# Kernel optimization log

Measured on AMD Instinct MI355X. Metric: run time of the kernel, lower is better.

Reference implementation:

```python
import jax, jax.numpy as jnp
import numpy as np

B = 8192
H_IN = 128
H = 512
Z = 128
N = 512   # must equal H due to W_up(h,h) -> W_down(n,.) chaining in the source
RW = 16
TEMP = 0.666
EPS = 1e-20


def _xavier(key, shape):
    fan_in, fan_out = shape[0], shape[1]
    lim = float(np.sqrt(6.0 / (fan_in + fan_out)))
    return jax.random.uniform(key, shape, jnp.float32, -lim, lim)


def setup_inputs() -> dict:
    key = jax.random.key(0)
    ks = jax.random.split(key, 24)
    inp = {
        'latent': jax.random.normal(ks[0], (B, Z), jnp.float32),
        'inputs': jnp.zeros((B, H_IN), jnp.float32),
        'gumbel_u': jax.random.uniform(ks[1], (RW, B, N), jnp.float32),
        # weights stored [in, out] for x @ W
        'W_int': _xavier(ks[2], (Z, H)),   'b_int': jnp.zeros((H,), jnp.float32),
        'W_intl': _xavier(ks[3], (Z, H)),  'b_intl': jnp.zeros((H,), jnp.float32),
        'W_hup': _xavier(ks[4], (H, H)),   'b_hup': jnp.zeros((H,), jnp.float32),
        'W_cup': _xavier(ks[5], (H, H)),   'b_cup': jnp.zeros((H,), jnp.float32),
        'W_hupl': _xavier(ks[6], (H, H)),  'b_hupl': jnp.zeros((H,), jnp.float32),
        'W_cupl': _xavier(ks[7], (H, H)),  'b_cupl': jnp.zeros((H,), jnp.float32),
        'W_lstm': _xavier(ks[8], (H_IN + H, 4 * H)), 'b_lstm': jnp.zeros((4 * H,), jnp.float32),
        'W_up': _xavier(ks[9], (H, H)),    'b_up': jnp.zeros((H,), jnp.float32),
        'W_down': _xavier(ks[10], (N, H_IN)),        # no bias
        'W_downl': _xavier(ks[11], (N, H_IN)),       # no bias
        'W_outl': _xavier(ks[12], (H, 1)), 'b_outl': jnp.zeros((1,), jnp.float32),
    }
    return inp


def _lstm_step(x, hx, cx, W_lstm, b_lstm):
    gates = jnp.concatenate([x, hx], axis=1) @ W_lstm + b_lstm  # [B, 4H]
    i, g, f, o = jnp.split(gates, 4, axis=1)
    cy = cx * jax.nn.sigmoid(f + 1.0) + jax.nn.sigmoid(i) * jnp.tanh(g)
    hy = jax.nn.sigmoid(o) * jnp.tanh(cy)
    return hy, cy


def _forward(latent, inputs, gumbel_u,
             W_int, b_int, W_intl, b_intl,
             W_hup, b_hup, W_cup, b_cup,
             W_hupl, b_hupl, W_cupl, b_cupl,
             W_lstm, b_lstm, W_up, b_up,
             W_down, W_downl, W_outl, b_outl):
    inter = jnp.tanh(latent @ W_int + b_int)
    hx = jnp.tanh(inter @ W_hup + b_hup)
    cx = jnp.tanh(inter @ W_cup + b_cup)
    inter_l = jnp.tanh(latent @ W_intl + b_intl)
    hxl = jnp.tanh(inter_l @ W_hupl + b_hupl)
    cxl = jnp.tanh(inter_l @ W_cupl + b_cupl)

    def step1(carry, u):
        x, h, c = carry
        hy, cy = _lstm_step(x, h, c, W_lstm, b_lstm)
        logits = hy @ W_up + b_up                       # [B, N]
        g = -jnp.log(-jnp.log(u + EPS) + EPS)           # gumbel noise
        y = jax.nn.softmax((logits + g) / TEMP, axis=1)
        y_hard = (y == jnp.max(y, axis=1, keepdims=True)).astype(y.dtype)
        y = jax.lax.stop_gradient(y_hard - y) + y       # straight-through hard sample
        return (y @ W_down, hy, cy), y

    _, out_steps = jax.lax.scan(step1, (inputs, hx, cx), gumbel_u)  # [RW, B, N]

    def step2(carry, y):
        h, c = carry
        xl = y @ W_downl
        hy, cy = _lstm_step(xl, h, c, W_lstm, b_lstm)   # source reuses lstm_cell here
        return (hy, cy), hy @ W_outl + b_outl           # [B, 1]

    _, line_steps = jax.lax.scan(step2, (hxl, cxl), out_steps)      # [RW, B, 1]

    return (jnp.transpose(out_steps, (1, 0, 2)),   # [B, RW, N]
            jnp.transpose(line_steps, (1, 0, 2)))  # [B, RW, 1]


def reference(latent, inputs, gumbel_u,
              W_int, b_int, W_intl, b_intl,
              W_hup, b_hup, W_cup, b_cup,
              W_hupl, b_hupl, W_cupl, b_cupl,
              W_lstm, b_lstm, W_up, b_up,
              W_down, W_downl, W_outl, b_outl):
    return _forward(latent, inputs, gumbel_u,
                    W_int, b_int, W_intl, b_intl,
                    W_hup, b_hup, W_cup, b_cup,
                    W_hupl, b_hupl, W_cupl, b_cupl,
                    W_lstm, b_lstm, W_up, b_up,
                    W_down, W_downl, W_outl, b_outl)
```

## Files before the change

### kernel.cpp

```cpp
#include <hip/hip_runtime.h>

#define NB 8192
#define NH 512
#define NZ 128
#define NIN 128
#define NN 512
#define NRW 16
#define NG 2048

typedef _Float16 f16;
typedef _Float16 f16x8 __attribute__((ext_vector_type(8)));
typedef float f32x4 __attribute__((ext_vector_type(4)));

__device__ __forceinline__ float sigm(float x) { return 1.0f / (1.0f + expf(-x)); }

__device__ __forceinline__ int oc_of(int c)
{
    return (((c >> 4) & 3) << 9) + ((c >> 6) << 4) + (c & 15);
}
__device__ __forceinline__ int cperm(int j)
{
    return (j & 15) | (((j >> 4) & 31) << 6) | (((j >> 9) & 3) << 4);
}

__device__ __forceinline__ void swz_xcd(int& bx, int& by)
{
    const int gx = gridDim.x;
    const int nwg = gx * gridDim.y;
    int lin = by * gx + bx;
    lin = (lin & 7) * (nwg >> 3) + (lin >> 3);
    const int sh = 31 - __clz(gx);
    bx = lin & (gx - 1);
    by = lin >> sh;
}

__device__ __forceinline__ void gload16(const f16* g, f16* l)
{
    __builtin_amdgcn_global_load_lds(
        (const __attribute__((address_space(1))) void*)g,
        (__attribute__((address_space(3))) void*)l, 16, 0, 0);
}

__device__ __forceinline__ int swz4(int row) { return (row & 3) ^ ((row >> 2) & 3); }

__device__ __forceinline__ void stage_tile(f16* tilebase, const f16* src,
                                           int rowbase, int kb, int wid, int lane)
{
#pragma unroll
    for (int q = 0; q < 2; ++q) {
        const int iw = wid * 2 + q;
        const int chunk = (iw << 6) | lane;
        const int row = chunk >> 2;
        const int p = (chunk & 3) ^ swz4(row);
        const f16* g = src + (size_t)(rowbase + row) * NH + kb + (p << 3);
        gload16(g, tilebase + (iw << 9));
    }
}

__device__ __forceinline__ f16x8 frag(const f16* tile, int row, int sl)
{
    return *(const f16x8*)(tile + row * 32 + ((sl ^ swz4(row)) << 3));
}

__device__ __forceinline__ void readA(f16x8 (&a)[4], const f16* sbuf, int wr, int r16, int sl)
{
#pragma unroll
    for (int f = 0; f < 4; ++f) a[f] = frag(sbuf, wr + f * 16 + r16, sl);
}

__device__ __forceinline__ void loadBfr(f16x8 (&d)[4], const f16* p, size_t base)
{
#pragma unroll
    for (int f = 0; f < 4; ++f) d[f] = *(const f16x8*)(p + base + f * 512);
}

__device__ __forceinline__ f32x4 MM(const f16x8 a, const f16x8 b, f32x4 c)
{
    return __builtin_amdgcn_mfma_f32_16x16x32_f16(a, b, c, 0, 0, 0);
}

template<int SPLIT>
__device__ __forceinline__ void core3(const f16* Ahi, const f16* Alo,
                                      const f16* Bph, const f16* Bpl,
                                      f16* s0h, f16* s0l, f16* s1h, f16* s1l,
                                      int bm, int bnblk, int wid, int lane, int wr, int wc2,
                                      f32x4 (&acc)[4][4])
{
    const int r16 = lane & 15, sl = lane >> 4;
    const size_t bwoff = (size_t)(wc2 << 11) + lane * 8;
    f16x8 bAh[4], bAl[4], bBh[4], bBl[4];

    stage_tile(s0h, Ahi, bm, 0, wid, lane);
    if (SPLIT) stage_tile(s0l, Alo, bm, 0, wid, lane);
    loadBfr(bAh, Bph, (((size_t)bnblk << 4) << 12) + bwoff);
    if (SPLIT) loadBfr(bAl, Bpl, (((size_t)bnblk << 4) << 12) + bwoff);

#pragma unroll 1
    for (int kt = 0; kt < 16; kt += 2) {
        __syncthreads();
        {
            const int kn = kt + 1;
            stage_tile(s1h, Ahi, bm, kn << 5, wid, lane);
            if (SPLIT) stage_tile(s1l, Alo, bm, kn << 5, wid, lane);
            loadBfr(bBh, Bph, ((((size_t)bnblk << 4) + kn) << 12) + bwoff);
            if (SPLIT) loadBfr(bBl, Bpl, ((((size_t)bnblk << 4) + kn) << 12) + bwoff);
        }
        f16x8 ah[4], al[4];
        readA(ah, s0h, wr, r16, sl);
        if (SPLIT) readA(al, s0l, wr, r16, sl);
        __builtin_amdgcn_s_setprio(1);
#pragma unroll
        for (int i = 0; i < 4; ++i)
#pragma unroll
            for (int j = 0; j < 4; ++j) {
                acc[i][j] = MM(ah[i], bAh[j], acc[i][j]);
                if (SPLIT) {
                    acc[i][j] = MM(al[i], bAh[j], acc[i][j]);
                    acc[i][j] = MM(ah[i], bAl[j], acc[i][j]);
                }
            }
        __builtin_amdgcn_s_setprio(0);
        __syncthreads();
        if (kt + 2 < 16) {
            const int kn = kt + 2;
            stage_tile(s0h, Ahi, bm, kn << 5, wid, lane);
            if (SPLIT) stage_tile(s0l, Alo, bm, kn << 5, wid, lane);
            loadBfr(bAh, Bph, ((((size_t)bnblk << 4) + kn) << 12) + bwoff);
            if (SPLIT) loadBfr(bAl, Bpl, ((((size_t)bnblk << 4) + kn) << 12) + bwoff);
        }
        readA(ah, s1h, wr, r16, sl);
        if (SPLIT) readA(al, s1l, wr, r16, sl);
        __builtin_amdgcn_s_setprio(1);
#pragma unroll
        for (int i = 0; i < 4; ++i)
#pragma unroll
            for (int j = 0; j < 4; ++j) {
                acc[i][j] = MM(ah[i], bBh[j], acc[i][j]);
                if (SPLIT) {
                    acc[i][j] = MM(al[i], bBh[j], acc[i][j]);
                    acc[i][j] = MM(ah[i], bBl[j], acc[i][j]);
                }
            }
        __builtin_amdgcn_s_setprio(0);
    }
}

template<int OUT>
__global__ __launch_bounds__(256, 2)
void mfma_gemm(const f16* __restrict__ Ahi, const f16* __restrict__ Alo,
               const f16* __restrict__ Bph, const f16* __restrict__ Bpl,
               const float* __restrict__ bias,
               float* __restrict__ C, f16* __restrict__ Ohi, f16* __restrict__ Olo)
{
    __shared__ f16 s[4][4096];
    int bx = blockIdx.x, by = blockIdx.y;
    swz_xcd(bx, by);
    const int bm = by << 7;
    const int tid = threadIdx.x;
    const int wid = tid >> 6, lane = tid & 63;
    const int wr = ((wid >> 1) & 1) << 6;
    const int wc2 = wid & 1;

    f32x4 acc[4][4];
#pragma unroll
    for (int i = 0; i < 4; ++i)
#pragma unroll
        for (int j = 0; j < 4; ++j) acc[i][j] = (f32x4)(0.0f);

    core3<1>(Ahi, Alo, Bph, Bpl, s[0], s[1], s[2], s[3], bm, bx, wid, lane, wr, wc2, acc);

    const int r16 = lane & 15, rg = lane >> 4;
#pragma unroll
    for (int i = 0; i < 4; ++i) {
#pragma unroll
        for (int r = 0; r < 4; ++r) {
            const int row = bm + wr + i * 16 + rg * 4 + r;
#pragma unroll
            for (int j = 0; j < 4; ++j) {
                const int col = (bx << 7) + (wc2 << 6) + j * 16 + r16;
                float v = acc[i][j][r] + bias[col];
                v = tanhf(v);
                const size_t idx = (size_t)row * NH + col;
                if (OUT == 1) C[idx] = v;
                else {
                    const f16 a = (f16)v;
                    Ohi[idx] = a;
                    if (OUT == 2) Olo[idx] = (f16)(v - (float)a);
                }
            }
        }
    }
}

__global__ __launch_bounds__(256, 2)
void mfma_logits_argmax(const f16* __restrict__ Ahi, const f16* __restrict__ Alo,
                        const f16* __restrict__ Bph, const f16* __restrict__ Bpl,
                        const float* __restrict__ bias,
                        const float* __restrict__ gu,
                        float2* __restrict__ part, int t)
{
    __shared__ f16 s[4][4096];
    int bx = blockIdx.x, by = blockIdx.y;
    swz_xcd(bx, by);
    const int bm = by << 7;
    const int tid = threadIdx.x;
    const int wid = tid >> 6, lane = tid & 63;
    const int wr = ((wid >> 1) & 1) << 6;
    const int wc2 = wid & 1;

    f32x4 acc[4][4];
#pragma unroll
    for (int i = 0; i < 4; ++i)
#pragma unroll
        for (int j = 0; j < 4; ++j) acc[i][j] = (f32x4)(0.0f);

    core3<1>(Ahi, Alo, Bph, Bpl, s[0], s[1], s[2], s[3], bm, bx, wid, lane, wr, wc2, acc);

    const int r16 = lane & 15, rg = lane >> 4;
    const int cb = (bx << 1) + wc2;
    float bi[4];
#pragma unroll
    for (int j = 0; j < 4; ++j) bi[j] = bias[(bx << 7) + (wc2 << 6) + j * 16 + r16];

#pragma unroll
    for (int i = 0; i < 4; ++i) {
#pragma unroll
        for (int r = 0; r < 4; ++r) {
            const int row = bm + wr + i * 16 + rg * 4 + r;
            const float* urow = gu + ((size_t)t * NB + row) * NN;
            float best = -INFINITY;
            int bidx = 0x7fffffff;
#pragma unroll
            for (int j = 0; j < 4; ++j) {
                const int col = (bx << 7) + (wc2 << 6) + j * 16 + r16;
                const float u = urow[col];
                const float g = -logf(-logf(u + 1e-20f) + 1e-20f);
                const float v = acc[i][j][r] + bi[j] + g;
                if (v > best || (v == best && col < bidx)) { best = v; bidx = col; }
            }
#pragma unroll
            for (int msk = 1; msk < 16; msk <<= 1) {
                const float ov = __shfl_xor(best, msk);
                const int oi = __shfl_xor(bidx, msk);
                if (ov > best || (ov == best && oi < bidx)) { best = ov; bidx = oi; }
            }
            if (r16 == 0) part[(size_t)row * 8 + cb] = make_float2(best, (float)bidx);
        }
    }
}

__global__ __launch_bounds__(256)
void finalize_argmax(const float2* __restrict__ part,
                     float* __restrict__ out0, int* __restrict__ kidx, int t)
{
    const int w = threadIdx.x >> 6;
    const int lane = threadIdx.x & 63;
    const int row = blockIdx.x * 4 + w;
    float best = -INFINITY;
    int bi = 0x7fffffff;
    if (lane < 8) {
        const float2 p = part[(size_t)row * 8 + lane];
        best = p.x;
        bi = (int)p.y;
    }
#pragma unroll
    for (int msk = 1; msk < 8; msk <<= 1) {
        const float ov = __shfl_xor(best, msk);
        const int oi = __shfl_xor(bi, msk);
        if (ov > best || (ov == best && oi < bi)) { best = ov; bi = oi; }
    }
    const int win = __shfl(bi, 0);
    if (lane == 0) kidx[(size_t)t * NB + row] = win;
    float* orow = out0 + ((size_t)row * NRW + t) * NN;
    const int c0 = lane * 8;
    *(float4*)(orow + c0) = make_float4(c0 == win, c0 + 1 == win, c0 + 2 == win, c0 + 3 == win);
    *(float4*)(orow + c0 + 4) = make_float4(c0 + 4 == win, c0 + 5 == win, c0 + 6 == win, c0 + 7 == win);
}

template<int HAS_PART>
__global__ __launch_bounds__(256, 2)
void mfma_gate_lstm(const f16* __restrict__ Ahi, const f16* __restrict__ Alo,
                    const f16* __restrict__ Bph, const f16* __restrict__ Bpl,
                    const float* __restrict__ blp,
                    const float* __restrict__ extra,
                    const float2* __restrict__ part,
                    int* __restrict__ kidx, float* __restrict__ out0, int t,
                    float* __restrict__ c,
                    f16* __restrict__ h_hi, f16* __restrict__ h_lo)
{
    __shared__ f16 s[4][4096];
    __shared__ int winlds[128];
    int bx = blockIdx.x, by = blockIdx.y;
    swz_xcd(bx, by);
    const int bm = by << 7;
    const int tid = threadIdx.x;
    const int wid = tid >> 6, lane = tid & 63;
    const int wr = ((wid >> 1) & 1) << 6;
    const int wc2 = wid & 1;

    if (HAS_PART && tid < 128) {
        const float2* p = part + (size_t)(bm + tid) * 8;
        float best = -INFINITY;
        int bi = 0x7fffffff;
#pragma unroll
        for (int q = 0; q < 8; ++q) {
            const float2 pv = p[q];
            if (pv.x > best || (pv.x == best && (int)pv.y < bi)) { best = pv.x; bi = (int)pv.y; }
        }
        winlds[tid] = bi;
        if (bx == 0) kidx[(size_t)(t - 1) * NB + bm + tid] = bi;
    }

    f32x4 acc[4][4];
#pragma unroll
    for (int i = 0; i < 4; ++i)
#pragma unroll
        for (int j = 0; j < 4; ++j) acc[i][j] = (f32x4)(0.0f);

    core3<1>(Ahi, Alo, Bph, Bpl, s[0], s[1], s[2], s[3], bm, bx, wid, lane, wr, wc2, acc);

    const int m = lane & 15, rg = lane >> 4;
    const int colb = (bx << 7) + (wc2 << 6);
    const int jj = ((colb >> 6) << 4) + m;
    float bi4[4];
#pragma unroll
    for (int g = 0; g < 4; ++g) bi4[g] = blp[colb + g * 16 + m];

#pragma unroll
    for (int i = 0; i < 4; ++i) {
#pragma unroll
        for (int r = 0; r < 4; ++r) {
            const int row = bm + wr + i * 16 + rg * 4 + r;
            float ex[4] = {0.f, 0.f, 0.f, 0.f};
            if (HAS_PART) {
                const float* exr = extra + (size_t)winlds[row - bm] * NG;
#pragma unroll
                for (int g = 0; g < 4; ++g) ex[g] = exr[colb + g * 16 + m];
            }
            const float ig = acc[i][0][r] + bi4[0] + ex[0];
            const float gg = acc[i][1][r] + bi4[1] + ex[1];
            const float fg = acc[i][2][r] + bi4[2] + ex[2];
            const float og = acc[i][3][r] + bi4[3] + ex[3];
            const size_t cidx = (size_t)row * NH + jj;
            const float cx = c[cidx];
            const float cy = cx * sigm(fg + 1.0f) + sigm(ig) * tanhf(gg);
            const float hy = sigm(og) * tanhf(cy);
            c[cidx] = cy;
            const f16 a = (f16)hy;
            h_hi[cidx] = a;
            h_lo[cidx] = (f16)(hy - (float)a);
        }
    }

    if (HAS_PART) {
        const int rr = tid >> 1;
        const int cs = (bx << 5) + ((tid & 1) << 4);
        const int win = winlds[rr];
        float* orow = out0 + ((size_t)(bm + rr) * NRW + (t - 1)) * NN + cs;
#pragma unroll
        for (int e = 0; e < 16; e += 4) {
            const int c0 = cs + e;
            *(float4*)(orow + e) = make_float4(c0 == win, c0 + 1 == win, c0 + 2 == win, c0 + 3 == win);
        }
    }
}

__global__ __launch_bounds__(256, 3)
void mfma_gate_lstm2(const f16* __restrict__ Ahi, const f16* __restrict__ Bph,
                     const float* __restrict__ blp,
                     const float* __restrict__ extra, const int* __restrict__ eidx,
                     float* __restrict__ c,
                     f16* __restrict__ h_hi,
                     const float* __restrict__ Woutl,
                     float* __restrict__ out1, int t)
{
    __shared__ f16 s[2][4096];
    int bx = blockIdx.x, by = blockIdx.y;
    swz_xcd(bx, by);
    const int bm = by << 7;
    const int tid = threadIdx.x;
    const int wid = tid >> 6, lane = tid & 63;
    const int wr = ((wid >> 1) & 1) << 6;
    const int wc2 = wid & 1;

    f32x4 acc[4][4];
#pragma unroll
    for (int i = 0; i < 4; ++i)
#pragma unroll
        for (int j = 0; j < 4; ++j) acc[i][j] = (f32x4)(0.0f);

    core3<0>(Ahi, nullptr, Bph, nullptr, s[0], nullptr, s[1], nullptr,
             bm, bx, wid, lane, wr, wc2, acc);

    const int m = lane & 15, rg = lane >> 4;
    const int colb = (bx << 7) + (wc2 << 6);
    const int jj = ((colb >> 6) << 4) + m;
    const float wout = Woutl[jj];
    float bi4[4];
#pragma unroll
    for (int g = 0; g < 4; ++g) bi4[g] = blp[colb + g * 16 + m];

#pragma unroll
    for (int i = 0; i < 4; ++i) {
#pragma unroll
        for (int r = 0; r < 4; ++r) {
            const int row = bm + wr + i * 16 + rg * 4 + r;
            const float* exr = extra + (size_t)eidx[row] * NG;
            float ex[4];
#pragma unroll
            for (int g = 0; g < 4; ++g) ex[g] = exr[colb + g * 16 + m];
            const float ig = acc[i][0][r] + bi4[0] + ex[0];
            const float gg = acc[i][1][r] + bi4[1] + ex[1];
            const float fg = acc[i][2][r] + bi4[2] + ex[2];
            const float og = acc[i][3][r] + bi4[3] + ex[3];
            const size_t cidx = (size_t)row * NH + jj;
            const float cx = c[cidx];
            const float cy = cx * sigm(fg + 1.0f) + sigm(ig) * tanhf(gg);
            const float hy = sigm(og) * tanhf(cy);
            c[cidx] = cy;
            h_hi[cidx] = (f16)hy;
            float pt = hy * wout;
#pragma unroll
            for (int msk = 1; msk < 16; msk <<= 1) pt += __shfl_xor(pt, msk);
            if (m == 0) atomicAdd(&out1[(size_t)row * NRW + t], pt);
        }
    }
}

__global__ __launch_bounds__(256)
void out1_init(float* __restrict__ out1, const float* __restrict__ boutl)
{
    const size_t i = (size_t)blockIdx.x * 256 + threadIdx.x;
    out1[i] = boutl[0];
}

template<int ACT, int PERM>
__global__ __launch_bounds__(256)
void gemm128(const float* __restrict__ A, int lda,
             const float* __restrict__ W, int ldw,
             const float* __restrict__ bias,
             float* __restrict__ C, int ldc, int K)
{
    __shared__ float As[16][128];
    __shared__ float Bs[16][128];
    const int bm = blockIdx.y << 7, bn = blockIdx.x << 7;
    const int tid = threadIdx.x;
    const int tx = tid & 15, ty = tid >> 4;
    const int sar = tid >> 1, sac = (tid & 1) << 3;
    const int sbk = tid >> 4, sbc = (tid & 15) << 3;
    float acc[2][2][4][4] = {};
    const float* Ap = A + (size_t)(bm + sar) * lda + sac;
    const float* Wp = W + (size_t)sbk * ldw + bn + sbc;
    for (int kb = 0; kb < K; kb += 16) {
        const float4 av0 = *(const float4*)(Ap + kb);
        const float4 av1 = *(const float4*)(Ap + kb + 4);
        const float4 bv0 = *(const float4*)(Wp + (size_t)kb * ldw);
        const float4 bv1 = *(const float4*)(Wp + (size_t)kb * ldw + 4);
        __syncthreads();
        As[sac + 0][sar] = av0.x; As[sac + 1][sar] = av0.y;
        As[sac + 2][sar] = av0.z; As[sac + 3][sar] = av0.w;
        As[sac + 4][sar] = av1.x; As[sac + 5][sar] = av1.y;
        As[sac + 6][sar] = av1.z; As[sac + 7][sar] = av1.w;
        *(float4*)&Bs[sbk][sbc] = bv0;
        *(float4*)&Bs[sbk][sbc + 4] = bv1;
        __syncthreads();
#pragma unroll
        for (int kk = 0; kk < 16; ++kk) {
            float a[2][4], b[2][4];
            *(float4*)a[0] = *(const float4*)&As[kk][ty << 2];
            *(float4*)a[1] = *(const float4*)&As[kk][64 + (ty << 2)];
            *(float4*)b[0] = *(const float4*)&Bs[kk][tx << 2];
            *(float4*)b[1] = *(const float4*)&Bs[kk][64 + (tx << 2)];
#pragma unroll
            for (int rh = 0; rh < 2; ++rh)
#pragma unroll
                for (int ch = 0; ch < 2; ++ch)
#pragma unroll
                    for (int i = 0; i < 4; ++i)
#pragma unroll
                        for (int j = 0; j < 4; ++j)
                            acc[rh][ch][i][j] = fmaf(a[rh][i], b[ch][j], acc[rh][ch][i][j]);
        }
    }
    float4 bi4[2] = {make_float4(0.f, 0.f, 0.f, 0.f), make_float4(0.f, 0.f, 0.f, 0.f)};
    if (bias) {
        bi4[0] = *(const float4*)(bias + bn + (tx << 2));
        bi4[1] = *(const float4*)(bias + bn + 64 + (tx << 2));
    }
#pragma unroll
    for (int rh = 0; rh < 2; ++rh)
#pragma unroll
        for (int i = 0; i < 4; ++i) {
            const int row = bm + rh * 64 + (ty << 2) + i;
#pragma unroll
            for (int ch = 0; ch < 2; ++ch) {
                const int col = bn + ch * 64 + (tx << 2);
                float v0 = acc[rh][ch][i][0] + bi4[ch].x;
                float v1 = acc[rh][ch][i][1] + bi4[ch].y;
                float v2 = acc[rh][ch][i][2] + bi4[ch].z;
                float v3 = acc[rh][ch][i][3] + bi4[ch].w;
                if (ACT == 1) { v0 = tanhf(v0); v1 = tanhf(v1); v2 = tanhf(v2); v3 = tanhf(v3); }
                const int wcol = PERM ? cperm(col) : col;
                *(float4*)(C + (size_t)row * ldc + wcol) = make_float4(v0, v1, v2, v3);
            }
        }
}

template<int PERM>
__global__ __launch_bounds__(256)
void tsplit_pack(const float* __restrict__ in, int ldin,
                 f16* __restrict__ phi, f16* __restrict__ plo)
{
    const int kt = blockIdx.x;
    const int nblk = blockIdx.y;
#pragma unroll
    for (int q = 0; q < 2; ++q) {
        const int cch = threadIdx.x + q * 256;
        const int wc2 = cch >> 8, f = (cch >> 6) & 3, slc = (cch >> 4) & 3, r16 = cch & 15;
        const int n = (nblk << 7) + (wc2 << 6) + (f << 4) + r16;
        const int ncol = PERM ? oc_of(n) : n;
        const int k0 = (kt << 5) + (slc << 3);
        f16x8 h8, l8;
#pragma unroll
        for (int e = 0; e < 8; ++e) {
            const float v = in[(size_t)(k0 + e) * ldin + ncol];
            const f16 hi = (f16)v;
            h8[e] = hi;
            l8[e] = (f16)(v - (float)hi);
        }
        const size_t off = ((((size_t)nblk << 4) + kt) << 12) + (size_t)cch * 8;
        *(f16x8*)(phi + off) = h8;
        *(f16x8*)(plo + off) = l8;
    }
}

__global__ __launch_bounds__(256)
void permb(const float* __restrict__ b, float* __restrict__ bp)
{
    const int c = blockIdx.x * 256 + threadIdx.x;
    bp[c] = b[oc_of(c)];
}

__global__ __launch_bounds__(256)
void split_h(const float* __restrict__ h, f16* __restrict__ hi, f16* __restrict__ lo)
{
    const size_t i = (size_t)blockIdx.x * 256 + threadIdx.x;
    const float v = h[i];
    const f16 a = (f16)v;
    hi[i] = a;
    lo[i] = (f16)(v - (float)a);
}

extern "C" void kernel_launch(void* const* d_in, const int* in_sizes, int n_in,
                              void* d_out, int out_size, void* d_ws, size_t ws_size,
                              hipStream_t stream)
{
    const float* latent  = (const float*)d_in[0];
    const float* gu      = (const float*)d_in[2];
    const float* W_int   = (const float*)d_in[3];
    const float* b_int   = (const float*)d_in[4];
    const float* W_intl  = (const float*)d_in[5];
    const float* b_intl  = (const float*)d_in[6];
    const float* W_hup   = (const float*)d_in[7];
    const float* b_hup   = (const float*)d_in[8];
    const float* W_cup   = (const float*)d_in[9];
    const float* b_cup   = (const float*)d_in[10];
    const float* W_hupl  = (const float*)d_in[11];
    const float* b_hupl  = (const float*)d_in[12];
    const float* W_cupl  = (const float*)d_in[13];
    const float* b_cupl  = (const float*)d_in[14];
    const float* W_lstm  = (const float*)d_in[15];
    const float* b_lstm  = (const float*)d_in[16];
    const float* W_up    = (const float*)d_in[17];
    const float* b_up    = (const float*)d_in[18];
    const float* W_down  = (const float*)d_in[19];
    const float* W_downl = (const float*)d_in[20];
    const float* W_outl  = (const float*)d_in[21];
    const float* b_outl  = (const float*)d_in[22];

    float* out0 = (float*)d_out;
    float* out1 = out0 + (size_t)NB * NRW * NN;

    float* ws     = (float*)d_ws;
    float* c      = ws;
    float* logits = c + (size_t)NB * NH;
    float* gdown  = logits + (size_t)NB * NH;
    float* gdownl = gdown + (size_t)NN * NG;
    float* blp    = gdownl + (size_t)NN * NG;
    float2* part  = (float2*)(blp + NG);
    f16* fp = (f16*)(part + (size_t)NB * 8);
    f16* h_hi[2]; f16* h_lo[2];
    h_hi[0] = fp;                    fp += (size_t)NB * NH;
    h_lo[0] = fp;                    fp += (size_t)NB * NH;
    h_hi[1] = fp;                    fp += (size_t)NB * NH;
    h_lo[1] = fp;                    fp += (size_t)NB * NH;
    f16* i_hi   = fp;                fp += (size_t)NB * NH;
    f16* i_lo   = fp;                fp += (size_t)NB * NH;
    f16* Wlp_hi = fp;                fp += (size_t)NG * NH;
    f16* Wlp_lo = fp;                fp += (size_t)NG * NH;
    f16* Wup_hi = fp;                fp += (size_t)NN * NH;
    f16* Wup_lo = fp;                fp += (size_t)NN * NH;
    f16* Whp_hi = fp;                fp += (size_t)NH * NH;
    f16* Whp_lo = fp;                fp += (size_t)NH * NH;
    f16* Wcp_hi = fp;                fp += (size_t)NH * NH;
    f16* Wcp_lo = fp;                fp += (size_t)NH * NH;
    f16* Whlp_hi = fp;               fp += (size_t)NH * NH;
    f16* Whlp_lo = fp;               fp += (size_t)NH * NH;
    f16* Wclp_hi = fp;               fp += (size_t)NH * NH;
    f16* Wclp_lo = fp;               fp += (size_t)NH * NH;
    int* kidx = (int*)fp;

    const dim3 blk(256);
    const dim3 g_gates(NG / 128, NB / 128);
    const dim3 g_h(NH / 128, NB / 128);
    const dim3 g_pre(NG / 128, NN / 128);
    const dim3 g_sph(NB * NH / 256);

    tsplit_pack<1><<<dim3(16, NG / 128), blk, 0, stream>>>(W_lstm + (size_t)NIN * NG, NG, Wlp_hi, Wlp_lo);
    tsplit_pack<0><<<dim3(16, NN / 128), blk, 0, stream>>>(W_up, NH, Wup_hi, Wup_lo);
    tsplit_pack<0><<<dim3(16, NH / 128), blk, 0, stream>>>(W_hup, NH, Whp_hi, Whp_lo);
    tsplit_pack<0><<<dim3(16, NH / 128), blk, 0, stream>>>(W_cup, NH, Wcp_hi, Wcp_lo);
    tsplit_pack<0><<<dim3(16, NH / 128), blk, 0, stream>>>(W_hupl, NH, Whlp_hi, Whlp_lo);
    tsplit_pack<0><<<dim3(16, NH / 128), blk, 0, stream>>>(W_cupl, NH, Wclp_hi, Wclp_lo);
    permb<<<dim3(NG / 256), blk, 0, stream>>>(b_lstm, blp);
    gemm128<0, 1><<<g_pre, blk, 0, stream>>>(W_down, NIN, W_lstm, NG, nullptr, gdown, NG, NIN);
    gemm128<0, 1><<<g_pre, blk, 0, stream>>>(W_downl, NIN, W_lstm, NG, nullptr, gdownl, NG, NIN);

    gemm128<1, 0><<<g_h, blk, 0, stream>>>(latent, NZ, W_int, NH, b_int, logits, NH, NZ);
    split_h<<<g_sph, blk, 0, stream>>>(logits, i_hi, i_lo);
    mfma_gemm<2><<<g_h, blk, 0, stream>>>(i_hi, i_lo, Whp_hi, Whp_lo, b_hup,
                                          nullptr, h_hi[0], h_lo[0]);
    mfma_gemm<1><<<g_h, blk, 0, stream>>>(i_hi, i_lo, Wcp_hi, Wcp_lo, b_cup,
                                          c, nullptr, nullptr);

    int cur = 0;
    for (int t = 0; t < NRW; ++t) {
        const int nxt = cur ^ 1;
        if (t == 0)
            mfma_gate_lstm<0><<<g_gates, blk, 0, stream>>>(h_hi[cur], h_lo[cur], Wlp_hi, Wlp_lo,
                                                           blp, nullptr, nullptr, nullptr, nullptr, t,
                                                           c, h_hi[nxt], h_lo[nxt]);
        else
            mfma_gate_lstm<1><<<g_gates, blk, 0, stream>>>(h_hi[cur], h_lo[cur], Wlp_hi, Wlp_lo,
                                                           blp, gdown, part, kidx, out0, t,
                                                           c, h_hi[nxt], h_lo[nxt]);
        mfma_logits_argmax<<<g_h, blk, 0, stream>>>(h_hi[nxt], h_lo[nxt], Wup_hi, Wup_lo,
                                                    b_up, gu, part, t);
        cur = nxt;
    }
    finalize_argmax<<<dim3(NB / 4), blk, 0, stream>>>(part, out0, kidx, NRW - 1);

    gemm128<1, 0><<<g_h, blk, 0, stream>>>(latent, NZ, W_intl, NH, b_intl, logits, NH, NZ);
    split_h<<<g_sph, blk, 0, stream>>>(logits, i_hi, i_lo);
    mfma_gemm<3><<<g_h, blk, 0, stream>>>(i_hi, i_lo, Whlp_hi, Whlp_lo, b_hupl,
                                          nullptr, h_hi[0], nullptr);
    mfma_gemm<1><<<g_h, blk, 0, stream>>>(i_hi, i_lo, Wclp_hi, Wclp_lo, b_cupl,
                                          c, nullptr, nullptr);
    out1_init<<<dim3(NB * NRW / 256), blk, 0, stream>>>(out1, b_outl);

    cur = 0;
    for (int t = 0; t < NRW; ++t) {
        const int nxt = cur ^ 1;
        mfma_gate_lstm2<<<g_gates, blk, 0, stream>>>(h_hi[cur], Wlp_hi,
                                                     blp, gdownl, kidx + (size_t)t * NB,
                                                     c, h_hi[nxt],
                                                     W_outl, out1, t);
        cur = nxt;
    }
}
```

Measured before the change: 2.882 ms.

## Interleave second LSTM recurrence with first via fused dual-layer gate kernel

The second (line) LSTM scan now runs in the same launch as the first scan's next step, using a z-dimension of 2 in a new fused_gate kernel. The step-2 gate at time t reads the argmax winner from the partial buffer directly, so the kidx buffer and the separate finalize pass go away. Setup work is also batched: weight packing, the gdown GEMMs, the input GEMMs with split, and the four init GEMMs each become one launch with a z-dimension. This halves the number of serialized recurrent launches and fills the GPU better, at the cost of a more complex kernel with branch divergence between block types and mixed split and non-split GEMM work in one grid.

```diff
diff --git a/kernel.cpp b/kernel.cpp
--- a/kernel.cpp
+++ b/kernel.cpp
@@ -145,148 +145,18 @@
     }
 }
 
-template<int OUT>
+template<int DO_L1, int DO_L2>
 __global__ __launch_bounds__(256, 2)
-void mfma_gemm(const f16* __restrict__ Ahi, const f16* __restrict__ Alo,
-               const f16* __restrict__ Bph, const f16* __restrict__ Bpl,
-               const float* __restrict__ bias,
-               float* __restrict__ C, f16* __restrict__ Ohi, f16* __restrict__ Olo)
-{
-    __shared__ f16 s[4][4096];
-    int bx = blockIdx.x, by = blockIdx.y;
-    swz_xcd(bx, by);
-    const int bm = by << 7;
-    const int tid = threadIdx.x;
-    const int wid = tid >> 6, lane = tid & 63;
-    const int wr = ((wid >> 1) & 1) << 6;
-    const int wc2 = wid & 1;
-
-    f32x4 acc[4][4];
-#pragma unroll
-    for (int i = 0; i < 4; ++i)
-#pragma unroll
-        for (int j = 0; j < 4; ++j) acc[i][j] = (f32x4)(0.0f);
-
-    core3<1>(Ahi, Alo, Bph, Bpl, s[0], s[1], s[2], s[3], bm, bx, wid, lane, wr, wc2, acc);
-
-    const int r16 = lane & 15, rg = lane >> 4;
-#pragma unroll
-    for (int i = 0; i < 4; ++i) {
-#pragma unroll
-        for (int r = 0; r < 4; ++r) {
-            const int row = bm + wr + i * 16 + rg * 4 + r;
-#pragma unroll
-            for (int j = 0; j < 4; ++j) {
-                const int col = (bx << 7) + (wc2 << 6) + j * 16 + r16;
-                float v = acc[i][j][r] + bias[col];
-                v = tanhf(v);
-                const size_t idx = (size_t)row * NH + col;
-                if (OUT == 1) C[idx] = v;
-                else {
-                    const f16 a = (f16)v;
-                    Ohi[idx] = a;
-                    if (OUT == 2) Olo[idx] = (f16)(v - (float)a);
-                }
-            }
-        }
-    }
-}
-
-__global__ __launch_bounds__(256, 2)
-void mfma_logits_argmax(const f16* __restrict__ Ahi, const f16* __restrict__ Alo,
-                        const f16* __restrict__ Bph, const f16* __restrict__ Bpl,
-                        const float* __restrict__ bias,
-                        const float* __restrict__ gu,
-                        float2* __restrict__ part, int t)
-{
-    __shared__ f16 s[4][4096];
-    int bx = blockIdx.x, by = blockIdx.y;
-    swz_xcd(bx, by);
-    const int bm = by << 7;
-    const int tid = threadIdx.x;
-    const int wid = tid >> 6, lane = tid & 63;
-    const int wr = ((wid >> 1) & 1) << 6;
-    const int wc2 = wid & 1;
-
-    f32x4 acc[4][4];
-#pragma unroll
-    for (int i = 0; i < 4; ++i)
-#pragma unroll
-        for (int j = 0; j < 4; ++j) acc[i][j] = (f32x4)(0.0f);
-
-    core3<1>(Ahi, Alo, Bph, Bpl, s[0], s[1], s[2], s[3], bm, bx, wid, lane, wr, wc2, acc);
-
-    const int r16 = lane & 15, rg = lane >> 4;
-    const int cb = (bx << 1) + wc2;
-    float bi[4];
-#pragma unroll
-    for (int j = 0; j < 4; ++j) bi[j] = bias[(bx << 7) + (wc2 << 6) + j * 16 + r16];
-
-#pragma unroll
-    for (int i = 0; i < 4; ++i) {
-#pragma unroll
-        for (int r = 0; r < 4; ++r) {
-            const int row = bm + wr + i * 16 + rg * 4 + r;
-            const float* urow = gu + ((size_t)t * NB + row) * NN;
-            float best = -INFINITY;
-            int bidx = 0x7fffffff;
-#pragma unroll
-            for (int j = 0; j < 4; ++j) {
-                const int col = (bx << 7) + (wc2 << 6) + j * 16 + r16;
-                const float u = urow[col];
-                const float g = -logf(-logf(u + 1e-20f) + 1e-20f);
-                const float v = acc[i][j][r] + bi[j] + g;
-                if (v > best || (v == best && col < bidx)) { best = v; bidx = col; }
-            }
-#pragma unroll
-            for (int msk = 1; msk < 16; msk <<= 1) {
-                const float ov = __shfl_xor(best, msk);
-                const int oi = __shfl_xor(bidx, msk);
-                if (ov > best || (ov == best && oi < bidx)) { best = ov; bidx = oi; }
-            }
-            if (r16 == 0) part[(size_t)row * 8 + cb] = make_float2(best, (float)bidx);
-        }
-    }
-}
-
-__global__ __launch_bounds__(256)
-void finalize_argmax(const float2* __restrict__ part,
-                     float* __restrict__ out0, int* __restrict__ kidx, int t)
-{
-    const int w = threadIdx.x >> 6;
-    const int lane = threadIdx.x & 63;
-    const int row = blockIdx.x * 4 + w;
-    float best = -INFINITY;
-    int bi = 0x7fffffff;
-    if (lane < 8) {
-        const float2 p = part[(size_t)row * 8 + lane];
-        best = p.x;
-        bi = (int)p.y;
-    }
-#pragma unroll
-    for (int msk = 1; msk < 8; msk <<= 1) {
-        const float ov = __shfl_xor(best, msk);
-        const int oi = __shfl_xor(bi, msk);
-        if (ov > best || (ov == best && oi < bi)) { best = ov; bi = oi; }
-    }
-    const int win = __shfl(bi, 0);
-    if (lane == 0) kidx[(size_t)t * NB + row] = win;
-    float* orow = out0 + ((size_t)row * NRW + t) * NN;
-    const int c0 = lane * 8;
-    *(float4*)(orow + c0) = make_float4(c0 == win, c0 + 1 == win, c0 + 2 == win, c0 + 3 == win);
-    *(float4*)(orow + c0 + 4) = make_float4(c0 + 4 == win, c0 + 5 == win, c0 + 6 == win, c0 + 7 == win);
-}
-
-template<int HAS_PART>
-__global__ __launch_bounds__(256, 2)
-void mfma_gate_lstm(const f16* __restrict__ Ahi, const f16* __restrict__ Alo,
-                    const f16* __restrict__ Bph, const f16* __restrict__ Bpl,
-                    const float* __restrict__ blp,
-                    const float* __restrict__ extra,
-                    const float2* __restrict__ part,
-                    int* __restrict__ kidx, float* __restrict__ out0, int t,
-                    float* __restrict__ c,
-                    f16* __restrict__ h_hi, f16* __restrict__ h_lo)
+void fused_gate(const f16* __restrict__ a1hi, const f16* __restrict__ a1lo,
+                const f16* __restrict__ a2hi,
+                const f16* __restrict__ Wlp_hi, const f16* __restrict__ Wlp_lo,
+                const float* __restrict__ blp,
+                const float* __restrict__ gdown, const float* __restrict__ gdownl,
+                const float2* __restrict__ part,
+                float* __restrict__ out0, int t_out,
+                float* __restrict__ c1, f16* __restrict__ o1hi, f16* __restrict__ o1lo,
+                float* __restrict__ c2, f16* __restrict__ o2hi,
+                const float* __restrict__ Woutl, float* __restrict__ out1, int t2)
 {
     __shared__ f16 s[4][4096];
     __shared__ int winlds[128];
@@ -297,8 +167,9 @@
     const int wid = tid >> 6, lane = tid & 63;
     const int wr = ((wid >> 1) & 1) << 6;
     const int wc2 = wid & 1;
-
-    if (HAS_PART && tid < 128) {
+    const bool isL1 = DO_L1 && (!DO_L2 || blockIdx.z == 0);
+
+    if (part != nullptr && tid < 128) {
         const float2* p = part + (size_t)(bm + tid) * 8;
         float best = -INFINITY;
         int bi = 0x7fffffff;
@@ -308,7 +179,6 @@
             if (pv.x > best || (pv.x == best && (int)pv.y < bi)) { best = pv.x; bi = (int)pv.y; }
         }
         winlds[tid] = bi;
-        if (bx == 0) kidx[(size_t)(t - 1) * NB + bm + tid] = bi;
     }
 
     f32x4 acc[4][4];
@@ -316,8 +186,6 @@
     for (int i = 0; i < 4; ++i)
 #pragma unroll
         for (int j = 0; j < 4; ++j) acc[i][j] = (f32x4)(0.0f);
-
-    core3<1>(Ahi, Alo, Bph, Bpl, s[0], s[1], s[2], s[3], bm, bx, wid, lane, wr, wc2, acc);
 
     const int m = lane & 15, rg = lane >> 4;
     const int colb = (bx << 7) + (wc2 << 6);
@@ -326,55 +194,96 @@
 #pragma unroll
     for (int g = 0; g < 4; ++g) bi4[g] = blp[colb + g * 16 + m];
 
-#pragma unroll
-    for (int i = 0; i < 4; ++i) {
-#pragma unroll
-        for (int r = 0; r < 4; ++r) {
-            const int row = bm + wr + i * 16 + rg * 4 + r;
-            float ex[4] = {0.f, 0.f, 0.f, 0.f};
-            if (HAS_PART) {
-                const float* exr = extra + (size_t)winlds[row - bm] * NG;
+    if (isL1) {
+        core3<1>(a1hi, a1lo, Wlp_hi, Wlp_lo, s[0], s[1], s[2], s[3],
+                 bm, bx, wid, lane, wr, wc2, acc);
+#pragma unroll
+        for (int i = 0; i < 4; ++i) {
+#pragma unroll
+            for (int r = 0; r < 4; ++r) {
+                const int row = bm + wr + i * 16 + rg * 4 + r;
+                float ex[4] = {0.f, 0.f, 0.f, 0.f};
+                if (part != nullptr) {
+                    const float* exr = gdown + (size_t)winlds[row - bm] * NG;
+#pragma unroll
+                    for (int g = 0; g < 4; ++g) ex[g] = exr[colb + g * 16 + m];
+                }
+                const float ig = acc[i][0][r] + bi4[0] + ex[0];
+                const float gg = acc[i][1][r] + bi4[1] + ex[1];
+                const float fg = acc[i][2][r] + bi4[2] + ex[2];
+                const float og = acc[i][3][r] + bi4[3] + ex[3];
+                const size_t cidx = (size_t)row * NH + jj;
+                const float cx = c1[cidx];
+                const float cy = cx * sigm(fg + 1.0f) + sigm(ig) * tanhf(gg);
+                const float hy = sigm(og) * tanhf(cy);
+                c1[cidx] = cy;
+                const f16 a = (f16)hy;
+                o1hi[cidx] = a;
+                o1lo[cidx] = (f16)(hy - (float)a);
+            }
+        }
+        if (part != nullptr) {
+            const int rr = tid >> 1;
+            const int cs = (bx << 5) + ((tid & 1) << 4);
+            const int win = winlds[rr];
+            float* orow = out0 + ((size_t)(bm + rr) * NRW + t_out) * NN + cs;
+#pragma unroll
+            for (int e = 0; e < 16; e += 4) {
+                const int c0 = cs + e;
+                *(float4*)(orow + e) = make_float4(c0 == win, c0 + 1 == win, c0 + 2 == win, c0 + 3 == win);
+            }
+        }
+    } else {
+        core3<0>(a2hi, nullptr, Wlp_hi, nullptr, s[0], nullptr, s[1], nullptr,
+                 bm, bx, wid, lane, wr, wc2, acc);
+        const float wout = Woutl[jj];
+#pragma unroll
+        for (int i = 0; i < 4; ++i) {
+#pragma unroll
+            for (int r = 0; r < 4; ++r) {
+                const int row = bm + wr + i * 16 + rg * 4 + r;
+                const float* exr = gdownl + (size_t)winlds[row - bm] * NG;
+                float ex[4];
 #pragma unroll
                 for (int g = 0; g < 4; ++g) ex[g] = exr[colb + g * 16 + m];
-            }
-            const float ig = acc[i][0][r] + bi4[0] + ex[0];
-            const float gg = acc[i][1][r] + bi4[1] + ex[1];
-            const float fg = acc[i][2][r] + bi4[2] + ex[2];
-            const float og = acc[i][3][r] + bi4[3] + ex[3];
-            const size_t cidx = (size_t)row * NH + jj;
-            const float cx = c[cidx];
-            const float cy = cx * sigm(fg + 1.0f) + sigm(ig) * tanhf(gg);
-            const float hy = sigm(og) * tanhf(cy);
-            c[cidx] = cy;
-            const f16 a = (f16)hy;
-            h_hi[cidx] = a;
-            h_lo[cidx] = (f16)(hy - (float)a);
-        }
-    }
-
-    if (HAS_PART) {
-        const int rr = tid >> 1;
-        const int cs = (bx << 5) + ((tid & 1) << 4);
-        const int win = winlds[rr];
-        float* orow = out0 + ((size_t)(bm + rr) * NRW + (t - 1)) * NN + cs;
-#pragma unroll
-        for (int e = 0; e < 16; e += 4) {
-            const int c0 = cs + e;
-            *(float4*)(orow + e) = make_float4(c0 == win, c0 + 1 == win, c0 + 2 == win, c0 + 3 == win);
-        }
-    }
-}
-
-__global__ __launch_bounds__(256, 3)
-void mfma_gate_lstm2(const f16* __restrict__ Ahi, const f16* __restrict__ Bph,
-                     const float* __restrict__ blp,
-                     const float* __restrict__ extra, const int* __restrict__ eidx,
-                     float* __restrict__ c,
-                     f16* __restrict__ h_hi,
-                     const float* __restrict__ Woutl,
-                     float* __restrict__ out1, int t)
-{
-    __shared__ f16 s[2][4096];
+                const float ig = acc[i][0][r] + bi4[0] + ex[0];
+                const float gg = acc[i][1][r] + bi4[1] + ex[1];
+                const float fg = acc[i][2][r] + bi4[2] + ex[2];
+                const float og = acc[i][3][r] + bi4[3] + ex[3];
+                const size_t cidx = (size_t)row * NH + jj;
+                const float cx = c2[cidx];
+                const float cy = cx * sigm(fg + 1.0f) + sigm(ig) * tanhf(gg);
+                const float hy = sigm(og) * tanhf(cy);
+                c2[cidx] = cy;
+                o2hi[cidx] = (f16)hy;
+                float pt = hy * wout;
+#pragma unroll
+                for (int msk = 1; msk < 16; msk <<= 1) pt += __shfl_xor(pt, msk);
+                if (m == 0) atomicAdd(&out1[(size_t)row * NRW + t2], pt);
+            }
+        }
+        if (!DO_L1) {
+            const int rr = tid >> 1;
+            const int cs = (bx << 5) + ((tid & 1) << 4);
+            const int win = winlds[rr];
+            float* orow = out0 + ((size_t)(bm + rr) * NRW + t_out) * NN + cs;
+#pragma unroll
+            for (int e = 0; e < 16; e += 4) {
+                const int c0 = cs + e;
+                *(float4*)(orow + e) = make_float4(c0 == win, c0 + 1 == win, c0 + 2 == win, c0 + 3 == win);
+            }
+        }
+    }
+}
+
+__global__ __launch_bounds__(256, 2)
+void mfma_logits_argmax(const f16* __restrict__ Ahi, const f16* __restrict__ Alo,
+                        const f16* __restrict__ Bph, const f16* __restrict__ Bpl,
+                        const float* __restrict__ bias,
+                        const float* __restrict__ gu,
+                        float2* __restrict__ part, int t)
+{
+    __shared__ f16 s[4][4096];
     int bx = blockIdx.x, by = blockIdx.y;
     swz_xcd(bx, by);
     const int bm = by << 7;
@@ -389,58 +298,113 @@
 #pragma unroll
         for (int j = 0; j < 4; ++j) acc[i][j] = (f32x4)(0.0f);
 
-    core3<0>(Ahi, nullptr, Bph, nullptr, s[0], nullptr, s[1], nullptr,
-             bm, bx, wid, lane, wr, wc2, acc);
-
-    const int m = lane & 15, rg = lane >> 4;
-    const int colb = (bx << 7) + (wc2 << 6);
-    const int jj = ((colb >> 6) << 4) + m;
-    const float wout = Woutl[jj];
-    float bi4[4];
-#pragma unroll
-    for (int g = 0; g < 4; ++g) bi4[g] = blp[colb + g * 16 + m];
+    core3<1>(Ahi, Alo, Bph, Bpl, s[0], s[1], s[2], s[3], bm, bx, wid, lane, wr, wc2, acc);
+
+    const int r16 = lane & 15, rg = lane >> 4;
+    const int cb = (bx << 1) + wc2;
+    float bi[4];
+#pragma unroll
+    for (int j = 0; j < 4; ++j) bi[j] = bias[(bx << 7) + (wc2 << 6) + j * 16 + r16];
 
 #pragma unroll
     for (int i = 0; i < 4; ++i) {
 #pragma unroll
         for (int r = 0; r < 4; ++r) {
             const int row = bm + wr + i * 16 + rg * 4 + r;
-            const float* exr = extra + (size_t)eidx[row] * NG;
-            float ex[4];
-#pragma unroll
-            for (int g = 0; g < 4; ++g) ex[g] = exr[colb + g * 16 + m];
-            const float ig = acc[i][0][r] + bi4[0] + ex[0];
-            const float gg = acc[i][1][r] + bi4[1] + ex[1];
-            const float fg = acc[i][2][r] + bi4[2] + ex[2];
-            const float og = acc[i][3][r] + bi4[3] + ex[3];
-            const size_t cidx = (size_t)row * NH + jj;
-            const float cx = c[cidx];
-            const float cy = cx * sigm(fg + 1.0f) + sigm(ig) * tanhf(gg);
-            const float hy = sigm(og) * tanhf(cy);
-            c[cidx] = cy;
-            h_hi[cidx] = (f16)hy;
-            float pt = hy * wout;
-#pragma unroll
-            for (int msk = 1; msk < 16; msk <<= 1) pt += __shfl_xor(pt, msk);
-            if (m == 0) atomicAdd(&out1[(size_t)row * NRW + t], pt);
+            const float* urow = gu + ((size_t)t * NB + row) * NN;
+            float best = -INFINITY;
+            int bidx = 0x7fffffff;
+#pragma unroll
+            for (int j = 0; j < 4; ++j) {
+                const int col = (bx << 7) + (wc2 << 6) + j * 16 + r16;
+                const float u = urow[col];
+                const float g = -logf(-logf(u + 1e-20f) + 1e-20f);
+                const float v = acc[i][j][r] + bi[j] + g;
+                if (v > best || (v == best && col < bidx)) { best = v; bidx = col; }
+            }
+#pragma unroll
+            for (int msk = 1; msk < 16; msk <<= 1) {
+                const float ov = __shfl_xor(best, msk);
+                const int oi = __shfl_xor(bidx, msk);
+                if (ov > best || (ov == best && oi < bidx)) { best = ov; bidx = oi; }
+            }
+            if (r16 == 0) part[(size_t)row * 8 + cb] = make_float2(best, (float)bidx);
+        }
+    }
+}
+
+__global__ __launch_bounds__(256, 2)
+void init4(const f16* __restrict__ i1hi, const f16* __restrict__ i1lo,
+           const f16* __restrict__ i2hi, const f16* __restrict__ i2lo,
+           const f16* __restrict__ Whp_hi, const f16* __restrict__ Whp_lo,
+           const f16* __restrict__ Wcp_hi, const f16* __restrict__ Wcp_lo,
+           const f16* __restrict__ Whlp_hi, const f16* __restrict__ Whlp_lo,
+           const f16* __restrict__ Wclp_hi, const f16* __restrict__ Wclp_lo,
+           const float* __restrict__ b_hup, const float* __restrict__ b_cup,
+           const float* __restrict__ b_hupl, const float* __restrict__ b_cupl,
+           float* __restrict__ c1, float* __restrict__ c2,
+           f16* __restrict__ h1hi, f16* __restrict__ h1lo, f16* __restrict__ h2hi)
+{
+    __shared__ f16 s[4][4096];
+    const int z = blockIdx.z;
+    const f16 *Ahi, *Alo, *Bh, *Bl;
+    const float* bias;
+    switch (z) {
+        case 0: Ahi = i1hi; Alo = i1lo; Bh = Whp_hi;  Bl = Whp_lo;  bias = b_hup;  break;
+        case 1: Ahi = i1hi; Alo = i1lo; Bh = Wcp_hi;  Bl = Wcp_lo;  bias = b_cup;  break;
+        case 2: Ahi = i2hi; Alo = i2lo; Bh = Whlp_hi; Bl = Whlp_lo; bias = b_hupl; break;
+        default: Ahi = i2hi; Alo = i2lo; Bh = Wclp_hi; Bl = Wclp_lo; bias = b_cupl; break;
+    }
+    int bx = blockIdx.x, by = blockIdx.y;
+    swz_xcd(bx, by);
+    const int bm = by << 7;
+    const int tid = threadIdx.x;
+    const int wid = tid >> 6, lane = tid & 63;
+    const int wr = ((wid >> 1) & 1) << 6;
+    const int wc2 = wid & 1;
+
+    f32x4 acc[4][4];
+#pragma unroll
+    for (int i = 0; i < 4; ++i)
+#pragma unroll
+        for (int j = 0; j < 4; ++j) acc[i][j] = (f32x4)(0.0f);
+
+    core3<1>(Ahi, Alo, Bh, Bl, s[0], s[1], s[2], s[3], bm, bx, wid, lane, wr, wc2, acc);
+
+    const int r16 = lane & 15, rg = lane >> 4;
+#pragma unroll
+    for (int i = 0; i < 4; ++i) {
+#pragma unroll
+        for (int r = 0; r < 4; ++r) {
+            const int row = bm + wr + i * 16 + rg * 4 + r;
+#pragma unroll
+            for (int j = 0; j < 4; ++j) {
+                const int col = (bx << 7) + (wc2 << 6) + j * 16 + r16;
+                float v = tanhf(acc[i][j][r] + bias[col]);
+                const size_t idx = (size_t)row * NH + col;
+                if (z == 0) {
+                    const f16 a = (f16)v;
+                    h1hi[idx] = a;
+                    h1lo[idx] = (f16)(v - (float)a);
+                } else if (z == 1) c1[idx] = v;
+                else if (z == 2) h2hi[idx] = (f16)v;
+                else c2[idx] = v;
+            }
         }
     }
 }
 
 __global__ __launch_bounds__(256)
-void out1_init(float* __restrict__ out1, const float* __restrict__ boutl)
-{
-    const size_t i = (size_t)blockIdx.x * 256 + threadIdx.x;
-    out1[i] = boutl[0];
-}
-
-template<int ACT, int PERM>
-__global__ __launch_bounds__(256)
-void gemm128(const float* __restrict__ A, int lda,
-             const float* __restrict__ W, int ldw,
-             const float* __restrict__ bias,
-             float* __restrict__ C, int ldc, int K)
-{
+void gemm128_split(const float* __restrict__ A,
+                   const float* __restrict__ W0, const float* __restrict__ b0,
+                   const float* __restrict__ W1, const float* __restrict__ b1,
+                   f16* __restrict__ o0hi, f16* __restrict__ o0lo,
+                   f16* __restrict__ o1hi, f16* __restrict__ o1lo)
+{
+    const float* W = blockIdx.z ? W1 : W0;
+    const float* bias = blockIdx.z ? b1 : b0;
+    f16* ohi = blockIdx.z ? o1hi : o0hi;
+    f16* olo = blockIdx.z ? o1lo : o0lo;
     __shared__ float As[16][128];
     __shared__ float Bs[16][128];
     const int bm = blockIdx.y << 7, bn = blockIdx.x << 7;
@@ -449,13 +413,13 @@
     const int sar = tid >> 1, sac = (tid & 1) << 3;
     const int sbk = tid >> 4, sbc = (tid & 15) << 3;
     float acc[2][2][4][4] = {};
-    const float* Ap = A + (size_t)(bm + sar) * lda + sac;
-    const float* Wp = W + (size_t)sbk * ldw + bn + sbc;
-    for (int kb = 0; kb < K; kb += 16) {
+    const float* Ap = A + (size_t)(bm + sar) * NZ + sac;
+    const float* Wp = W + (size_t)sbk * NH + bn + sbc;
+    for (int kb = 0; kb < NZ; kb += 16) {
         const float4 av0 = *(const float4*)(Ap + kb);
         const float4 av1 = *(const float4*)(Ap + kb + 4);
-        const float4 bv0 = *(const float4*)(Wp + (size_t)kb * ldw);
-        const float4 bv1 = *(const float4*)(Wp + (size_t)kb * ldw + 4);
+        const float4 bv0 = *(const float4*)(Wp + (size_t)kb * NH);
+        const float4 bv1 = *(const float4*)(Wp + (size_t)kb * NH + 4);
         __syncthreads();
         As[sac + 0][sar] = av0.x; As[sac + 1][sar] = av0.y;
         As[sac + 2][sar] = av0.z; As[sac + 3][sar] = av0.w;
@@ -482,11 +446,11 @@
                             acc[rh][ch][i][j] = fmaf(a[rh][i], b[ch][j], acc[rh][ch][i][j]);
         }
     }
-    float4 bi4[2] = {make_float4(0.f, 0.f, 0.f, 0.f), make_float4(0.f, 0.f, 0.f, 0.f)};
-    if (bias) {
-        bi4[0] = *(const float4*)(bias + bn + (tx << 2));
-        bi4[1] = *(const float4*)(bias + bn + 64 + (tx << 2));
-    }
+    float4 bi4[2];
+    bi4[0] = *(const float4*)(bias + bn + (tx << 2));
+    bi4[1] = *(const float4*)(bias + bn + 64 + (tx << 2));
+    const float bia[2][4] = {{bi4[0].x, bi4[0].y, bi4[0].z, bi4[0].w},
+                             {bi4[1].x, bi4[1].y, bi4[1].z, bi4[1].w}};
 #pragma unroll
     for (int rh = 0; rh < 2; ++rh)
 #pragma unroll
@@ -495,22 +459,106 @@
 #pragma unroll
             for (int ch = 0; ch < 2; ++ch) {
                 const int col = bn + ch * 64 + (tx << 2);
-                float v0 = acc[rh][ch][i][0] + bi4[ch].x;
-                float v1 = acc[rh][ch][i][1] + bi4[ch].y;
-                float v2 = acc[rh][ch][i][2] + bi4[ch].z;
-                float v3 = acc[rh][ch][i][3] + bi4[ch].w;
-                if (ACT == 1) { v0 = tanhf(v0); v1 = tanhf(v1); v2 = tanhf(v2); v3 = tanhf(v3); }
-                const int wcol = PERM ? cperm(col) : col;
-                *(float4*)(C + (size_t)row * ldc + wcol) = make_float4(v0, v1, v2, v3);
-            }
-        }
-}
-
-template<int PERM>
+#pragma unroll
+                for (int j = 0; j < 4; ++j) {
+                    const float v = tanhf(acc[rh][ch][i][j] + bia[ch][j]);
+                    const size_t idx = (size_t)row * NH + col + j;
+                    const f16 a = (f16)v;
+                    ohi[idx] = a;
+                    olo[idx] = (f16)(v - (float)a);
+                }
+            }
+        }
+}
+
 __global__ __launch_bounds__(256)
-void tsplit_pack(const float* __restrict__ in, int ldin,
-                 f16* __restrict__ phi, f16* __restrict__ plo)
-{
+void gemm128_gdown(const float* __restrict__ A0, const float* __restrict__ A1,
+                   const float* __restrict__ W,
+                   float* __restrict__ C0, float* __restrict__ C1)
+{
+    const float* A = blockIdx.z ? A1 : A0;
+    float* C = blockIdx.z ? C1 : C0;
+    __shared__ float As[16][128];
+    __shared__ float Bs[16][128];
+    const int bm = blockIdx.y << 7, bn = blockIdx.x << 7;
+    const int tid = threadIdx.x;
+    const int tx = tid & 15, ty = tid >> 4;
+    const int sar = tid >> 1, sac = (tid & 1) << 3;
+    const int sbk = tid >> 4, sbc = (tid & 15) << 3;
+    float acc[2][2][4][4] = {};
+    const float* Ap = A + (size_t)(bm + sar) * NIN + sac;
+    const float* Wp = W + (size_t)sbk * NG + bn + sbc;
+    for (int kb = 0; kb < NIN; kb += 16) {
+        const float4 av0 = *(const float4*)(Ap + kb);
+        const float4 av1 = *(const float4*)(Ap + kb + 4);
+        const float4 bv0 = *(const float4*)(Wp + (size_t)kb * NG);
+        const float4 bv1 = *(const float4*)(Wp + (size_t)kb * NG + 4);
+        __syncthreads();
+        As[sac + 0][sar] = av0.x; As[sac + 1][sar] = av0.y;
+        As[sac + 2][sar] = av0.z; As[sac + 3][sar] = av0.w;
+        As[sac + 4][sar] = av1.x; As[sac + 5][sar] = av1.y;
+        As[sac + 6][sar] = av1.z; As[sac + 7][sar] = av1.w;
+        *(float4*)&Bs[sbk][sbc] = bv0;
+        *(float4*)&Bs[sbk][sbc + 4] = bv1;
+        __syncthreads();
+#pragma unroll
+        for (int kk = 0; kk < 16; ++kk) {
+            float a[2][4], b[2][4];
+            *(float4*)a[0] = *(const float4*)&As[kk][ty << 2];
+            *(float4*)a[1] = *(const float4*)&As[kk][64 + (ty << 2)];
+            *(float4*)b[0] = *(const float4*)&Bs[kk][tx << 2];
+            *(float4*)b[1] = *(const float4*)&Bs[kk][64 + (tx << 2)];
+#pragma unroll
+            for (int rh = 0; rh < 2; ++rh)
+#pragma unroll
+                for (int ch = 0; ch < 2; ++ch)
+#pragma unroll
+                    for (int i = 0; i < 4; ++i)
+#pragma unroll
+                        for (int j = 0; j < 4; ++j)
+                            acc[rh][ch][i][j] = fmaf(a[rh][i], b[ch][j], acc[rh][ch][i][j]);
+        }
+    }
+#pragma unroll
+    for (int rh = 0; rh < 2; ++rh)
+#pragma unroll
+        for (int i = 0; i < 4; ++i) {
+            const int row = bm + rh * 64 + (ty << 2) + i;
+#pragma unroll
+            for (int ch = 0; ch < 2; ++ch) {
+                const int col = bn + ch * 64 + (tx << 2);
+                *(float4*)(C + (size_t)row * NG + cperm(col)) =
+                    make_float4(acc[rh][ch][i][0], acc[rh][ch][i][1],
+                                acc[rh][ch][i][2], acc[rh][ch][i][3]);
+            }
+        }
+}
+
+__global__ __launch_bounds__(256)
+void tsplit_pack_all(const float* __restrict__ Wl, const float* __restrict__ Wup,
+                     const float* __restrict__ Whp, const float* __restrict__ Wcp,
+                     const float* __restrict__ Whlp, const float* __restrict__ Wclp,
+                     f16* __restrict__ Wlp_hi, f16* __restrict__ Wlp_lo,
+                     f16* __restrict__ Wup_hi, f16* __restrict__ Wup_lo,
+                     f16* __restrict__ Whp_hi, f16* __restrict__ Whp_lo,
+                     f16* __restrict__ Wcp_hi, f16* __restrict__ Wcp_lo,
+                     f16* __restrict__ Whlp_hi, f16* __restrict__ Whlp_lo,
+                     f16* __restrict__ Wclp_hi, f16* __restrict__ Wclp_lo)
+{
+    const int z = blockIdx.z;
+    const int nblkcnt = (z == 0) ? 16 : 4;
+    if ((int)blockIdx.y >= nblkcnt) return;
+    const float* src;
+    int ldin, perm;
+    f16 *ph, *pl;
+    switch (z) {
+        case 0: src = Wl;   ldin = NG; perm = 1; ph = Wlp_hi;  pl = Wlp_lo;  break;
+        case 1: src = Wup;  ldin = NH; perm = 0; ph = Wup_hi;  pl = Wup_lo;  break;
+        case 2: src = Whp;  ldin = NH; perm = 0; ph = Whp_hi;  pl = Whp_lo;  break;
+        case 3: src = Wcp;  ldin = NH; perm = 0; ph = Wcp_hi;  pl = Wcp_lo;  break;
+        case 4: src = Whlp; ldin = NH; perm = 0; ph = Whlp_hi; pl = Whlp_lo; break;
+        default: src = Wclp; ldin = NH; perm = 0; ph = Wclp_hi; pl = Wclp_lo; break;
+    }
     const int kt = blockIdx.x;
     const int nblk = blockIdx.y;
 #pragma unroll
@@ -518,19 +566,19 @@
         const int cch = threadIdx.x + q * 256;
         const int wc2 = cch >> 8, f = (cch >> 6) & 3, slc = (cch >> 4) & 3, r16 = cch & 15;
         const int n = (nblk << 7) + (wc2 << 6) + (f << 4) + r16;
-        const int ncol = PERM ? oc_of(n) : n;
+        const int ncol = perm ? oc_of(n) : n;
         const int k0 = (kt << 5) + (slc << 3);
         f16x8 h8, l8;
 #pragma unroll
         for (int e = 0; e < 8; ++e) {
-            const float v = in[(size_t)(k0 + e) * ldin + ncol];
+            const float v = src[(size_t)(k0 + e) * ldin + ncol];
             const f16 hi = (f16)v;
             h8[e] = hi;
             l8[e] = (f16)(v - (float)hi);
         }
         const size_t off = ((((size_t)nblk << 4) + kt) << 12) + (size_t)cch * 8;
-        *(f16x8*)(phi + off) = h8;
-        *(f16x8*)(plo + off) = l8;
+        *(f16x8*)(ph + off) = h8;
+        *(f16x8*)(pl + off) = l8;
     }
 }
 
@@ -542,13 +590,10 @@
 }
 
 __global__ __launch_bounds__(256)
-void split_h(const float* __restrict__ h, f16* __restrict__ hi, f16* __restrict__ lo)
+void out1_init(float* __restrict__ out1, const float* __restrict__ boutl)
 {
     const size_t i = (size_t)blockIdx.x * 256 + threadIdx.x;
-    const float v = h[i];
-    const f16 a = (f16)v;
-    hi[i] = a;
-    lo[i] = (f16)(v - (float)a);
+    out1[i] = boutl[0];
 }
 
 extern "C" void kernel_launch(void* const* d_in, const int* in_sizes, int n_in,
@@ -582,20 +627,24 @@
     float* out1 = out0 + (size_t)NB * NRW * NN;
 
     float* ws     = (float*)d_ws;
-    float* c      = ws;
-    float* logits = c + (size_t)NB * NH;
-    float* gdown  = logits + (size_t)NB * NH;
+    float* c1     = ws;
+    float* c2     = c1 + (size_t)NB * NH;
+    float* gdown  = c2 + (size_t)NB * NH;
     float* gdownl = gdown + (size_t)NN * NG;
     float* blp    = gdownl + (size_t)NN * NG;
     float2* part  = (float2*)(blp + NG);
     f16* fp = (f16*)(part + (size_t)NB * 8);
-    f16* h_hi[2]; f16* h_lo[2];
-    h_hi[0] = fp;                    fp += (size_t)NB * NH;
-    h_lo[0] = fp;                    fp += (size_t)NB * NH;
-    h_hi[1] = fp;                    fp += (size_t)NB * NH;
-    h_lo[1] = fp;                    fp += (size_t)NB * NH;
-    f16* i_hi   = fp;                fp += (size_t)NB * NH;
-    f16* i_lo   = fp;                fp += (size_t)NB * NH;
+    f16* h1hi[2]; f16* h1lo[2]; f16* h2hi[2];
+    h1hi[0] = fp;                    fp += (size_t)NB * NH;
+    h1lo[0] = fp;                    fp += (size_t)NB * NH;
+    h1hi[1] = fp;                    fp += (size_t)NB * NH;
+    h1lo[1] = fp;                    fp += (size_t)NB * NH;
+    h2hi[0] = fp;                    fp += (size_t)NB * NH;
+    h2hi[1] = fp;                    fp += (size_t)NB * NH;
+    f16* i1hi = fp;                  fp += (size_t)NB * NH;
+    f16* i1lo = fp;                  fp += (size_t)NB * NH;
+    f16* i2hi = fp;                  fp += (size_t)NB * NH;
+    f16* i2lo = fp;                  fp += (size_t)NB * NH;
     f16* Wlp_hi = fp;                fp += (size_t)NG * NH;
     f16* Wlp_lo = fp;                fp += (size_t)NG * NH;
     f16* Wup_hi = fp;                fp += (size_t)NN * NH;
@@ -608,63 +657,54 @@
     f16* Whlp_lo = fp;               fp += (size_t)NH * NH;
     f16* Wclp_hi = fp;               fp += (size_t)NH * NH;
     f16* Wclp_lo = fp;               fp += (size_t)NH * NH;
-    int* kidx = (int*)fp;
 
     const dim3 blk(256);
-    const dim3 g_gates(NG / 128, NB / 128);
-    const dim3 g_h(NH / 128, NB / 128);
-    const dim3 g_pre(NG / 128, NN / 128);
-    const dim3 g_sph(NB * NH / 256);
-
-    tsplit_pack<1><<<dim3(16, NG / 128), blk, 0, stream>>>(W_lstm + (size_t)NIN * NG, NG, Wlp_hi, Wlp_lo);
-    tsplit_pack<0><<<dim3(16, NN / 128), blk, 0, stream>>>(W_up, NH, Wup_hi, Wup_lo);
-    tsplit_pack<0><<<dim3(16, NH / 128), blk, 0, stream>>>(W_hup, NH, Whp_hi, Whp_lo);
-    tsplit_pack<0><<<dim3(16, NH / 128), blk, 0, stream>>>(W_cup, NH, Wcp_hi, Wcp_lo);
-    tsplit_pack<0><<<dim3(16, NH / 128), blk, 0, stream>>>(W_hupl, NH, Whlp_hi, Whlp_lo);
-    tsplit_pack<0><<<dim3(16, NH / 128), blk, 0, stream>>>(W_cupl, NH, Wclp_hi, Wclp_lo);
+
+    tsplit_pack_all<<<dim3(16, 16, 6), blk, 0, stream>>>(
+        W_lstm + (size_t)NIN * NG, W_up, W_hup, W_cup, W_hupl, W_cupl,
+        Wlp_hi, Wlp_lo, Wup_hi, Wup_lo, Whp_hi, Whp_lo, Wcp_hi, Wcp_lo,
+        Whlp_hi, Whlp_lo, Wclp_hi, Wclp_lo);
     permb<<<dim3(NG / 256), blk, 0, stream>>>(b_lstm, blp);
-    gemm128<0, 1><<<g_pre, blk, 0, stream>>>(W_down, NIN, W_lstm, NG, nullptr, gdown, NG, NIN);
-    gemm128<0, 1><<<g_pre, blk, 0, stream>>>(W_downl, NIN, W_lstm, NG, nullptr, gdownl, NG, NIN);
-
-    gemm128<1, 0><<<g_h, blk, 0, stream>>>(latent, NZ, W_int, NH, b_int, logits, NH, NZ);
-    split_h<<<g_sph, blk, 0, stream>>>(logits, i_hi, i_lo);
-    mfma_gemm<2><<<g_h, blk, 0, stream>>>(i_hi, i_lo, Whp_hi, Whp_lo, b_hup,
-                                          nullptr, h_hi[0], h_lo[0]);
-    mfma_gemm<1><<<g_h, blk, 0, stream>>>(i_hi, i_lo, Wcp_hi, Wcp_lo, b_cup,
-                                          c, nullptr, nullptr);
-
-    int cur = 0;
-    for (int t = 0; t < NRW; ++t) {
-        const int nxt = cur ^ 1;
-        if (t == 0)
-            mfma_gate_lstm<0><<<g_gates, blk, 0, stream>>>(h_hi[cur], h_lo[cur], Wlp_hi, Wlp_lo,
-                                                           blp, nullptr, nullptr, nullptr, nullptr, t,
-                                                           c, h_hi[nxt], h_lo[nxt]);
-        else
-            mfma_gate_lstm<1><<<g_gates, blk, 0, stream>>>(h_hi[cur], h_lo[cur], Wlp_hi, Wlp_lo,
-                                                           blp, gdown, part, kidx, out0, t,
-                                                           c, h_hi[nxt], h_lo[nxt]);
-        mfma_logits_argmax<<<g_h, blk, 0, stream>>>(h_hi[nxt], h_lo[nxt], Wup_hi, Wup_lo,
-                                                    b_up, gu, part, t);
-        cur = nxt;
-    }
-    finalize_argmax<<<dim3(NB / 4), blk, 0, stream>>>(part, out0, kidx, NRW - 1);
-
-    gemm128<1, 0><<<g_h, blk, 0, stream>>>(latent, NZ, W_intl, NH, b_intl, logits, NH, NZ);
-    split_h<<<g_sph, blk, 0, stream>>>(logits, i_hi, i_lo);
-    mfma_gemm<3><<<g_h, blk, 0, stream>>>(i_hi, i_lo, Whlp_hi, Whlp_lo, b_hupl,
-                                          nullptr, h_hi[0], nullptr);
-    mfma_gemm<1><<<g_h, blk, 0, stream>>>(i_hi, i_lo, Wclp_hi, Wclp_lo, b_cupl,
-                                          c, nullptr, nullptr);
+    gemm128_gdown<<<dim3(NG / 128, NN / 128, 2), blk, 0, stream>>>(W_down, W_downl, W_lstm,
+                                                                   gdown, gdownl);
+    gemm128_split<<<dim3(NH / 128, NB / 128, 2), blk, 0, stream>>>(latent, W_int, b_int,
+                                                                   W_intl, b_intl,
+                                                                   i1hi, i1lo, i2hi, i2lo);
+    init4<<<dim3(NH / 128, NB / 128, 4), blk, 0, stream>>>(
+        i1hi, i1lo, i2hi, i2lo,
+        Whp_hi, Whp_lo, Wcp_hi, Wcp_lo, Whlp_hi, Whlp_lo, Wclp_hi, Wclp_lo,
+        b_hup, b_cup, b_hupl, b_cupl,
+        c1, c2, h1hi[0], h1lo[0], h2hi[0]);
     out1_init<<<dim3(NB * NRW / 256), blk, 0, stream>>>(out1, b_outl);
 
-    cur = 0;
-    for (int t = 0; t < NRW; ++t) {
-        const int nxt = cur ^ 1;
-        mfma_gate_lstm2<<<g_gates, blk, 0, stream>>>(h_hi[cur], Wlp_hi,
-                                                     blp, gdownl, kidx + (size_t)t * NB,
-                                                     c, h_hi[nxt],
-                                                     W_outl, out1, t);
-        cur = nxt;
-    }
-}
+    const dim3 g1(NG / 128, NB / 128, 1);
+    const dim3 g2(NG / 128, NB / 128, 2);
+    const dim3 gl(NN / 128, NB / 128);
+
+    fused_gate<1, 0><<<g1, blk, 0, stream>>>(h1hi[0], h1lo[0], nullptr,
+                                             Wlp_hi, Wlp_lo, blp, gdown, gdownl,
+                                             nullptr, out0, 0,
+                                             c1, h1hi[1], h1lo[1],
+                                             nullptr, nullptr, nullptr, nullptr, 0);
+    mfma_logits_argmax<<<gl, blk, 0, stream>>>(h1hi[1], h1lo[1], Wup_hi, Wup_lo,
+                                               b_up, gu, part, 0);
+
+    int c1i = 1, c2i = 0;
+    for (int t = 0; t < NRW - 1; ++t) {
+        const int n1 = c1i ^ 1, n2 = c2i ^ 1;
+        fused_gate<1, 1><<<g2, blk, 0, stream>>>(h1hi[c1i], h1lo[c1i], h2hi[c2i],
+                                                 Wlp_hi, Wlp_lo, blp, gdown, gdownl,
+                                                 part, out0, t,
+                                                 c1, h1hi[n1], h1lo[n1],
+                                                 c2, h2hi[n2], W_outl, out1, t);
+        mfma_logits_argmax<<<gl, blk, 0, stream>>>(h1hi[n1], h1lo[n1], Wup_hi, Wup_lo,
+                                                   b_up, gu, part, t + 1);
+        c1i = n1;
+        c2i = n2;
+    }
+    fused_gate<0, 1><<<g1, blk, 0, stream>>>(nullptr, nullptr, h2hi[c2i],
+                                             Wlp_hi, Wlp_lo, blp, gdown, gdownl,
+                                             part, out0, NRW - 1,
+                                             nullptr, nullptr, nullptr,
+                                             c2, h2hi[c2i ^ 1], W_outl, out1, NRW - 1);
+}
```

After: 2.759 ms. 1.04x faster.
